# Kernel optimization log

Hardware: AMD Instinct MI355X
Metric: run time of the kernel (lower is better)

## Reference

```python
import math
import jax, jax.numpy as jnp
import numpy as np

EMBED_LEN = 512  # self.dk in the torch module (used for scaling, NOT the head dim)


def setup_inputs() -> dict:
    key = jax.random.key(0)
    kq, kk, kv = jax.random.split(key, 3)
    B, H, S, D = 2, 8, 4096, 64
    queries = jax.random.normal(kq, (B, H, S, D), dtype=jnp.float32)
    keys = jax.random.normal(kk, (B, H, S, D), dtype=jnp.float32)
    # NOTE: values enters as [B, S, H, D]; forward transposes dims (1,2).
    values = jax.random.normal(kv, (B, S, H, D), dtype=jnp.float32)
    return {"queries": queries, "keys": keys, "values": values}


def reference(queries, keys, values):
    # compatibility = Q @ K^T / sqrt(dk), dk = embed_len (512), mask=None branch
    scores = jnp.einsum("bhqd,bhkd->bhqk", queries, keys) / math.sqrt(EMBED_LEN)
    attn = jax.nn.softmax(scores, axis=3)
    # torch.transpose(values, 1, 2): [B,S,H,D] -> [B,H,S,D]
    v = jnp.swapaxes(values, 1, 2)
    return jnp.einsum("bhqk,bhkd->bhqd", attn, v)
```

## Files before the change

### kernel.cpp

```cpp
#include <hip/hip_runtime.h>

typedef __attribute__((ext_vector_type(8))) short bf16x8;
typedef __attribute__((ext_vector_type(4))) short s16x4;
typedef __attribute__((ext_vector_type(4))) float f32x4;

#define MFMA16 __builtin_amdgcn_mfma_f32_16x16x32_bf16

#if __has_builtin(__builtin_amdgcn_exp2f)
__device__ __forceinline__ float exp2_raw(float x) { return __builtin_amdgcn_exp2f(x); }
#else
__device__ __forceinline__ float exp2_raw(float x) {
    float r;
    asm volatile("v_exp_f32 %0, %1" : "=v"(r) : "v"(x));
    return r;
}
#endif

__device__ __forceinline__ short bf16s(float f) {
    __bf16 h = (__bf16)f;
    return __builtin_bit_cast(short, h);
}

__device__ __forceinline__ void gload16(const char* g, char* l) {
    __builtin_amdgcn_global_load_lds(
        (const __attribute__((address_space(1))) unsigned int*)g,
        (__attribute__((address_space(3))) unsigned int*)l, 16, 0, 0);
}

__global__ __launch_bounds__(256) void prep_k(const float* __restrict__ K,
                                              char* __restrict__ Kimg) {
    const int bid = blockIdx.x;
    const int t = threadIdx.x;
    const int c = t & 3, r = t >> 2;
    char* dst = Kimg + (size_t)bid * 8192;
    const float* src = K + (size_t)bid * 4096 + (size_t)r * 64 + c * 16;
    float e[16];
    *(float4*)(e)      = *(const float4*)(src);
    *(float4*)(e + 4)  = *(const float4*)(src + 4);
    *(float4*)(e + 8)  = *(const float4*)(src + 8);
    *(float4*)(e + 12) = *(const float4*)(src + 12);
#pragma unroll
    for (int lg = 0; lg < 4; ++lg) {
        s16x4 wv;
#pragma unroll
        for (int j = 0; j < 4; ++j) wv[j] = bf16s(e[lg * 4 + j]);
        const unsigned f = (unsigned)((((c >> 1) * 4 + lg) ^ (r & 7)));
        *(s16x4*)(dst + r * 128 + f * 16 + (c & 1) * 8) = wv;
    }
}

__global__ __launch_bounds__(256) void prep_v(const float* __restrict__ V,
                                              char* __restrict__ Vimg) {
    const int bid = blockIdx.x;
    const int head = bid >> 6, it = bid & 63;
    const int b = head >> 3, h = head & 7;
    const int t = threadIdx.x;
    const int d = t & 63, f0 = t >> 6;
    char* dst = Vimg + (size_t)bid * 8192;
#pragma unroll
    for (int ff = 0; ff < 2; ++ff) {
        const int f = f0 + ff * 4;
        const int hh = f >> 2, lg = f & 3;
        const int kv0 = hh * 32 + lg * 4;
        const float* src = V + ((size_t)b * 4096 + it * 64 + kv0) * 512 + h * 64 + d;
        bf16x8 wv;
#pragma unroll
        for (int j = 0; j < 4; ++j) wv[j]     = bf16s(src[(size_t)j * 512]);
#pragma unroll
        for (int j = 0; j < 4; ++j) wv[4 + j] = bf16s(src[(size_t)(16 + j) * 512]);
        *(bf16x8*)(dst + d * 128 + (unsigned)((f ^ (d & 7)) * 16)) = wv;
    }
}

__global__ __launch_bounds__(64, 2)
void sdpa_fa_kernel(const float* __restrict__ Q, const char* __restrict__ Kimg,
                    const char* __restrict__ Vimg, float* __restrict__ P0,
                    float* __restrict__ P1, float* __restrict__ LS) {
    __shared__ __align__(16) char LDS[16384];

    const int bid  = blockIdx.x;
    const int xcd  = bid & 7;
    const int idx  = bid >> 3;
    const int head = xcd + 8 * (idx >> 7);
    const int kvh  = (idx >> 6) & 1;
    const int qt   = idx & 63;
    const int hb   = head * 64 + kvh * 32;

    const int l   = threadIdx.x;
    const int lg  = l >> 4;
    const int lc  = l & 15;
    const int lc7 = lc & 7;

    const float C1 = (float)(1.4426950408889634 / 22.627416997969522);

    bf16x8 qf[4][2];
#pragma unroll
    for (int qi = 0; qi < 4; ++qi) {
        const int qrow = qt * 64 + qi * 16 + lc;
        const float* qp = Q + ((size_t)head * 4096 + qrow) * 64;
#pragma unroll
        for (int half = 0; half < 2; ++half) {
            bf16x8 f;
#pragma unroll
            for (int j = 0; j < 4; ++j) {
                f[j]     = bf16s(qp[half * 32 + lg * 4 + j] * C1);
                f[4 + j] = bf16s(qp[half * 32 + 16 + lg * 4 + j] * C1);
            }
            qf[qi][half] = f;
        }
    }

    bf16x8 ones;
#pragma unroll
    for (int j = 0; j < 8; ++j) ones[j] = (short)0x3F80;

    f32x4 Oa[4][4];
    f32x4 ls[4];
#pragma unroll
    for (int qi = 0; qi < 4; ++qi) {
        ls[qi] = (f32x4){0.f, 0.f, 0.f, 0.f};
#pragma unroll
        for (int dt = 0; dt < 4; ++dt) Oa[qi][dt] = (f32x4){0.f, 0.f, 0.f, 0.f};
    }

    auto stage = [&](int it) {
        const char* gk = Kimg + (size_t)(hb + it) * 8192 + l * 16;
        const char* gv = Vimg + (size_t)(hb + it) * 8192 + l * 16;
#pragma unroll
        for (int i = 0; i < 8; ++i) gload16(gk + i * 1024, LDS + i * 1024);
#pragma unroll
        for (int i = 0; i < 8; ++i) gload16(gv + i * 1024, LDS + 8192 + i * 1024);
    };

    stage(0);

#pragma unroll 1
    for (int it = 0; it < 32; ++it) {
        asm volatile("s_waitcnt vmcnt(0)" ::: "memory");
        __builtin_amdgcn_sched_barrier(0);

        bf16x8 kf[4][2];
#pragma unroll
        for (int g = 0; g < 4; ++g) {
            const unsigned ro = (unsigned)((g * 16 + lc) * 128);
            kf[g][0] = *(const bf16x8*)(LDS + ro + (unsigned)(((0 + lg) ^ lc7) * 16));
            kf[g][1] = *(const bf16x8*)(LDS + ro + (unsigned)(((4 + lg) ^ lc7) * 16));
        }
        bf16x8 vf[4][2];
#pragma unroll
        for (int dt = 0; dt < 4; ++dt) {
            const unsigned ro = (unsigned)(8192 + (dt * 16 + lc) * 128);
            vf[dt][0] = *(const bf16x8*)(LDS + ro + (unsigned)(((0 + lg) ^ lc7) * 16));
            vf[dt][1] = *(const bf16x8*)(LDS + ro + (unsigned)(((4 + lg) ^ lc7) * 16));
        }
        asm volatile("s_waitcnt lgkmcnt(0)" ::: "memory");
        __builtin_amdgcn_sched_barrier(0);

        if (it + 1 < 32) stage(it + 1);
        __builtin_amdgcn_sched_barrier(0);

        f32x4 st0[4][2], st1[4][2];
#pragma unroll
        for (int g2 = 0; g2 < 2; ++g2)
#pragma unroll
            for (int qi = 0; qi < 4; ++qi) {
                f32x4 a = (f32x4){0.f, 0.f, 0.f, 0.f};
                a = MFMA16(kf[g2][0], qf[qi][0], a, 0, 0, 0);
                a = MFMA16(kf[g2][1], qf[qi][1], a, 0, 0, 0);
                st0[qi][g2] = a;
            }

#pragma unroll
        for (int g2 = 0; g2 < 2; ++g2)
#pragma unroll
            for (int qi = 0; qi < 4; ++qi) {
                f32x4 a = (f32x4){0.f, 0.f, 0.f, 0.f};
                a = MFMA16(kf[g2 + 2][0], qf[qi][0], a, 0, 0, 0);
                a = MFMA16(kf[g2 + 2][1], qf[qi][1], a, 0, 0, 0);
                st1[qi][g2] = a;
#pragma unroll
                for (int r = 0; r < 4; ++r) st0[qi][g2][r] = exp2_raw(st0[qi][g2][r]);
            }
        bf16x8 pfr0[4];
#pragma unroll
        for (int qi = 0; qi < 4; ++qi) {
            bf16x8 f;
#pragma unroll
            for (int j = 0; j < 4; ++j) {
                f[j]     = bf16s(st0[qi][0][j]);
                f[4 + j] = bf16s(st0[qi][1][j]);
            }
            pfr0[qi] = f;
        }

#pragma unroll
        for (int qi = 0; qi < 4; ++qi) {
            ls[qi] = MFMA16(pfr0[qi], ones, ls[qi], 0, 0, 0);
#pragma unroll
            for (int r = 0; r < 4; ++r) st1[qi][0][r] = exp2_raw(st1[qi][0][r]);
            Oa[qi][0] = MFMA16(pfr0[qi], vf[0][0], Oa[qi][0], 0, 0, 0);
            Oa[qi][1] = MFMA16(pfr0[qi], vf[1][0], Oa[qi][1], 0, 0, 0);
#pragma unroll
            for (int r = 0; r < 4; ++r) st1[qi][1][r] = exp2_raw(st1[qi][1][r]);
            Oa[qi][2] = MFMA16(pfr0[qi], vf[2][0], Oa[qi][2], 0, 0, 0);
            Oa[qi][3] = MFMA16(pfr0[qi], vf[3][0], Oa[qi][3], 0, 0, 0);
        }
        bf16x8 pfr1[4];
#pragma unroll
        for (int qi = 0; qi < 4; ++qi) {
            bf16x8 f;
#pragma unroll
            for (int j = 0; j < 4; ++j) {
                f[j]     = bf16s(st1[qi][0][j]);
                f[4 + j] = bf16s(st1[qi][1][j]);
            }
            pfr1[qi] = f;
        }

#pragma unroll
        for (int qi = 0; qi < 4; ++qi) {
            ls[qi] = MFMA16(pfr1[qi], ones, ls[qi], 0, 0, 0);
#pragma unroll
            for (int dt = 0; dt < 4; ++dt)
                Oa[qi][dt] = MFMA16(pfr1[qi], vf[dt][1], Oa[qi][dt], 0, 0, 0);
        }
    }

    float* P = kvh ? P1 : P0;
    float* lsw = LS + kvh * 65536;
#pragma unroll
    for (int qi = 0; qi < 4; ++qi) {
#pragma unroll
        for (int r = 0; r < 4; ++r) {
            const int q = qt * 64 + qi * 16 + lg * 4 + r;
            float* og = P + ((size_t)head * 4096 + q) * 64 + lc;
#pragma unroll
            for (int dt = 0; dt < 4; ++dt) og[dt * 16] = Oa[qi][dt][r];
            if (lc == 0) lsw[head * 4096 + q] = ls[qi][r];
        }
    }
}

__global__ __launch_bounds__(256) void merge_out(const float* __restrict__ P1,
                                                 const float* __restrict__ LS,
                                                 float* __restrict__ Out) {
    const int i = (blockIdx.x * 256 + threadIdx.x) * 4;
    const int hq = i >> 6;
    const float inv = 1.0f / (LS[hq] + LS[65536 + hq]);
    const float4 a = *(const float4*)(Out + i);
    const float4 b = *(const float4*)(P1 + i);
    float4 r;
    r.x = (a.x + b.x) * inv;
    r.y = (a.y + b.y) * inv;
    r.z = (a.z + b.z) * inv;
    r.w = (a.w + b.w) * inv;
    *(float4*)(Out + i) = r;
}

extern "C" void kernel_launch(void* const* d_in, const int* in_sizes, int n_in,
                              void* d_out, int out_size, void* d_ws, size_t ws_size,
                              hipStream_t stream) {
    const float* Q = (const float*)d_in[0];
    const float* K = (const float*)d_in[1];
    const float* V = (const float*)d_in[2];
    float* Out = (float*)d_out;
    char* Kimg = (char*)d_ws;
    char* Vimg = (char*)d_ws + (size_t)8388608;
    float* P1  = (float*)((char*)d_ws + (size_t)16777216);
    float* LS  = (float*)((char*)d_ws + (size_t)33554432);
    prep_k<<<dim3(1024), dim3(256), 0, stream>>>(K, Kimg);
    prep_v<<<dim3(1024), dim3(256), 0, stream>>>(V, Vimg);
    sdpa_fa_kernel<<<dim3(2048), dim3(64), 0, stream>>>(Q, Kimg, Vimg, Out, P1, LS);
    merge_out<<<dim3(4096), dim3(256), 0, stream>>>(P1, LS, Out);
}
```

Baseline: 93.90 us.

## Split K and V staging into separate pipelined loads with MFMA priority hints

Splits the per-iteration global-to-LDS staging into separate K and V loads, each waited on with a partial vmcnt. V fragments are now read just before the PV MFMAs and the next V tile is issued afterwards, so the V load overlaps the QK compute. LDS fragment offsets are precomputed outside the loop, and s_setprio raises wave priority around the MFMA blocks. The last iteration now issues a wasted wrapped-around prefetch of tile 0, and the partial vmcnt counting depends on exact load counts.

```diff
diff --git a/kernel.cpp b/kernel.cpp
--- a/kernel.cpp
+++ b/kernel.cpp
@@ -123,43 +123,48 @@
         for (int dt = 0; dt < 4; ++dt) Oa[qi][dt] = (f32x4){0.f, 0.f, 0.f, 0.f};
     }
 
-    auto stage = [&](int it) {
+    unsigned okf[4][2], ovf[4][2];
+#pragma unroll
+    for (int g = 0; g < 4; ++g) {
+        okf[g][0] = (unsigned)((g * 16 + lc) * 128 + (((0 + lg) ^ lc7) * 16));
+        okf[g][1] = (unsigned)((g * 16 + lc) * 128 + (((4 + lg) ^ lc7) * 16));
+        ovf[g][0] = (unsigned)(8192 + (g * 16 + lc) * 128 + (((0 + lg) ^ lc7) * 16));
+        ovf[g][1] = (unsigned)(8192 + (g * 16 + lc) * 128 + (((4 + lg) ^ lc7) * 16));
+    }
+
+    auto stage_k = [&](int it) {
         const char* gk = Kimg + (size_t)(hb + it) * 8192 + l * 16;
+#pragma unroll
+        for (int i = 0; i < 8; ++i) gload16(gk + i * 1024, LDS + i * 1024);
+    };
+    auto stage_v = [&](int it) {
         const char* gv = Vimg + (size_t)(hb + it) * 8192 + l * 16;
-#pragma unroll
-        for (int i = 0; i < 8; ++i) gload16(gk + i * 1024, LDS + i * 1024);
 #pragma unroll
         for (int i = 0; i < 8; ++i) gload16(gv + i * 1024, LDS + 8192 + i * 1024);
     };
 
-    stage(0);
+    stage_k(0);
+    stage_v(0);
 
 #pragma unroll 1
     for (int it = 0; it < 32; ++it) {
-        asm volatile("s_waitcnt vmcnt(0)" ::: "memory");
-        __builtin_amdgcn_sched_barrier(0);
-
+        const int nx = (it + 1) & 31;
+
+        asm volatile("s_waitcnt vmcnt(8)" ::: "memory");
+        __builtin_amdgcn_sched_barrier(0);
         bf16x8 kf[4][2];
 #pragma unroll
         for (int g = 0; g < 4; ++g) {
-            const unsigned ro = (unsigned)((g * 16 + lc) * 128);
-            kf[g][0] = *(const bf16x8*)(LDS + ro + (unsigned)(((0 + lg) ^ lc7) * 16));
-            kf[g][1] = *(const bf16x8*)(LDS + ro + (unsigned)(((4 + lg) ^ lc7) * 16));
-        }
-        bf16x8 vf[4][2];
-#pragma unroll
-        for (int dt = 0; dt < 4; ++dt) {
-            const unsigned ro = (unsigned)(8192 + (dt * 16 + lc) * 128);
-            vf[dt][0] = *(const bf16x8*)(LDS + ro + (unsigned)(((0 + lg) ^ lc7) * 16));
-            vf[dt][1] = *(const bf16x8*)(LDS + ro + (unsigned)(((4 + lg) ^ lc7) * 16));
+            kf[g][0] = *(const bf16x8*)(LDS + okf[g][0]);
+            kf[g][1] = *(const bf16x8*)(LDS + okf[g][1]);
         }
         asm volatile("s_waitcnt lgkmcnt(0)" ::: "memory");
         __builtin_amdgcn_sched_barrier(0);
-
-        if (it + 1 < 32) stage(it + 1);
+        stage_k(nx);
         __builtin_amdgcn_sched_barrier(0);
 
         f32x4 st0[4][2], st1[4][2];
+        __builtin_amdgcn_s_setprio(1);
 #pragma unroll
         for (int g2 = 0; g2 < 2; ++g2)
 #pragma unroll
@@ -169,7 +174,6 @@
                 a = MFMA16(kf[g2][1], qf[qi][1], a, 0, 0, 0);
                 st0[qi][g2] = a;
             }
-
 #pragma unroll
         for (int g2 = 0; g2 < 2; ++g2)
 #pragma unroll
@@ -181,6 +185,8 @@
 #pragma unroll
                 for (int r = 0; r < 4; ++r) st0[qi][g2][r] = exp2_raw(st0[qi][g2][r]);
             }
+        __builtin_amdgcn_s_setprio(0);
+
         bf16x8 pfr0[4];
 #pragma unroll
         for (int qi = 0; qi < 4; ++qi) {
@@ -193,6 +199,20 @@
             pfr0[qi] = f;
         }
 
+        asm volatile("s_waitcnt vmcnt(8)" ::: "memory");
+        __builtin_amdgcn_sched_barrier(0);
+        bf16x8 vf[4][2];
+#pragma unroll
+        for (int dt = 0; dt < 4; ++dt) {
+            vf[dt][0] = *(const bf16x8*)(LDS + ovf[dt][0]);
+            vf[dt][1] = *(const bf16x8*)(LDS + ovf[dt][1]);
+        }
+        asm volatile("s_waitcnt lgkmcnt(0)" ::: "memory");
+        __builtin_amdgcn_sched_barrier(0);
+        stage_v(nx);
+        __builtin_amdgcn_sched_barrier(0);
+
+        __builtin_amdgcn_s_setprio(1);
 #pragma unroll
         for (int qi = 0; qi < 4; ++qi) {
             ls[qi] = MFMA16(pfr0[qi], ones, ls[qi], 0, 0, 0);
@@ -205,6 +225,8 @@
             Oa[qi][2] = MFMA16(pfr0[qi], vf[2][0], Oa[qi][2], 0, 0, 0);
             Oa[qi][3] = MFMA16(pfr0[qi], vf[3][0], Oa[qi][3], 0, 0, 0);
         }
+        __builtin_amdgcn_s_setprio(0);
+
         bf16x8 pfr1[4];
 #pragma unroll
         for (int qi = 0; qi < 4; ++qi) {
@@ -217,6 +239,7 @@
             pfr1[qi] = f;
         }
 
+        __builtin_amdgcn_s_setprio(1);
 #pragma unroll
         for (int qi = 0; qi < 4; ++qi) {
             ls[qi] = MFMA16(pfr1[qi], ones, ls[qi], 0, 0, 0);
@@ -224,6 +247,7 @@
             for (int dt = 0; dt < 4; ++dt)
                 Oa[qi][dt] = MFMA16(pfr1[qi], vf[dt][1], Oa[qi][dt], 0, 0, 0);
         }
+        __builtin_amdgcn_s_setprio(0);
     }
 
     float* P = kvh ? P1 : P0;
```

After: 93.09 us. No clear change (-0.9%).
